# Kernel tuning notes

Hardware: AMD Instinct MI355X
Metric: run time of the kernel (lower is better)

## Reference

```python
import jax, jax.numpy as jnp
import numpy as np

B, S, V, D = 4, 2048, 50265, 768
H_LF, DH = 12, 64          # longformer-base heads
C, W = 256, 256            # chunk size, one-sided window
DFF = 3072
NH, DK = 4, 768            # outer MultiHeadAttention(n_head=4, d_k=d_v=768)


def layer_norm(x, g, b, eps=1e-5):
    mu = jnp.mean(x, axis=-1, keepdims=True)
    var = jnp.var(x, axis=-1, keepdims=True)
    return (x - mu) * jax.lax.rsqrt(var + eps) * g + b


def _overlap_chunks(t):
    # t: [B,H,S,dh] -> [B,H,nc,3c,dh] key blocks (chunks j-1,j,j+1, zero-padded at ends)
    nc = S // C
    tp = jnp.pad(t, ((0, 0), (0, 0), (C, C), (0, 0)))
    tr = tp.reshape(t.shape[0], t.shape[1], nc + 2, C, t.shape[-1])
    return jnp.concatenate([tr[:, :, :nc], tr[:, :, 1:nc + 1], tr[:, :, 2:]], axis=3)


def sliding_window_attn(q, k, v):
    # exact band attention: query i attends keys j with |i-j| <= W
    nc = S // C
    qc = q.reshape(q.shape[0], q.shape[1], nc, C, DH)
    kb = _overlap_chunks(k)
    vb = _overlap_chunks(v)
    scores = jnp.einsum('bhncd,bhnkd->bhnck', qc, kb) / np.sqrt(DH)
    ci = jnp.arange(C)[:, None]
    ki = jnp.arange(3 * C)[None, :]
    band = jnp.abs(ki - C - ci) <= W                      # [c,3c]
    n = jnp.arange(nc)[:, None]
    kpos = n * C - C + jnp.arange(3 * C)[None, :]
    valid = (kpos >= 0) & (kpos < S)                      # [nc,3c]
    mask = band[None, :, :] & valid[:, None, :]           # [nc,c,3c]
    scores = jnp.where(mask[None, None], scores, -1e9)
    a = jax.nn.softmax(scores, axis=-1)
    out = jnp.einsum('bhnck,bhnkd->bhncd', a, vb)
    return out.reshape(q.shape)


def longformer_layer(x, emb, pos, ln_e_g, ln_e_b, lf_wq, lf_wk, lf_wv, lf_wo,
                     ln1_g, ln1_b, w1, w2, ln2_g, ln2_b):
    h = layer_norm(emb[x] + pos[None], ln_e_g, ln_e_b)    # [B,S,D]
    def heads(w):
        return (h @ w).reshape(B, S, H_LF, DH).transpose(0, 2, 1, 3)
    q, k, v = heads(lf_wq), heads(lf_wk), heads(lf_wv)
    a = sliding_window_attn(q, k, v)                      # [B,H,S,dh]
    a = a.transpose(0, 2, 1, 3).reshape(B, S, D) @ lf_wo
    h = layer_norm(h + a, ln1_g, ln1_b)
    f = jax.nn.gelu(h @ w1) @ w2
    return layer_norm(h + f, ln2_g, ln2_b)


def mha_and_pool(x, out_lf, mha_wq, mha_wk, mha_wv, mha_fc, mha_ln_g, mha_ln_b):
    residual = out_lf
    def heads(w):
        return (out_lf @ w).reshape(B, S, NH, DK).transpose(0, 2, 1, 3)
    q, k, v = heads(mha_wq), heads(mha_wk), heads(mha_wv)
    scores = jnp.einsum('bhqd,bhkd->bhqk', q, k) / np.sqrt(DK)
    key_mask = (x != 0)[:, None, None, :]
    scores = jnp.where(key_mask, scores, -1e9)
    a = jax.nn.softmax(scores, axis=-1)
    o = jnp.einsum('bhqk,bhkd->bhqd', a, v)
    o = o.transpose(0, 2, 1, 3).reshape(B, S, NH * DK) @ mha_fc
    out_attn = layer_norm(o + residual, mha_ln_g, mha_ln_b)
    return jnp.max(out_attn, axis=1)                      # max_pool1d over seq -> [B,D]


def setup_inputs() -> dict:
    key = jax.random.key(0)
    ks = jax.random.split(key, 16)
    s = 0.02
    d = {
        'x': jax.random.randint(ks[0], (B, S), 0, V),
        'emb': jax.random.normal(ks[1], (V, D), jnp.float32) * s,
        'pos': jax.random.normal(ks[2], (S, D), jnp.float32) * s,
        'ln_e_g': jnp.ones((D,), jnp.float32), 'ln_e_b': jnp.zeros((D,), jnp.float32),
        'lf_wq': jax.random.normal(ks[3], (D, D), jnp.float32) * s,
        'lf_wk': jax.random.normal(ks[4], (D, D), jnp.float32) * s,
        'lf_wv': jax.random.normal(ks[5], (D, D), jnp.float32) * s,
        'lf_wo': jax.random.normal(ks[6], (D, D), jnp.float32) * s,
        'ln1_g': jnp.ones((D,), jnp.float32), 'ln1_b': jnp.zeros((D,), jnp.float32),
        'w1': jax.random.normal(ks[7], (D, DFF), jnp.float32) * s,
        'w2': jax.random.normal(ks[8], (DFF, D), jnp.float32) * s,
        'ln2_g': jnp.ones((D,), jnp.float32), 'ln2_b': jnp.zeros((D,), jnp.float32),
        'mha_wq': jax.random.normal(ks[9], (D, NH * DK), jnp.float32) * s,
        'mha_wk': jax.random.normal(ks[10], (D, NH * DK), jnp.float32) * s,
        'mha_wv': jax.random.normal(ks[11], (D, NH * DK), jnp.float32) * s,
        'mha_fc': jax.random.normal(ks[12], (NH * DK, D), jnp.float32) * s,
        'mha_ln_g': jnp.ones((D,), jnp.float32), 'mha_ln_b': jnp.zeros((D,), jnp.float32),
    }
    return d


def reference(x, emb, pos, ln_e_g, ln_e_b, lf_wq, lf_wk, lf_wv, lf_wo,
              ln1_g, ln1_b, w1, w2, ln2_g, ln2_b,
              mha_wq, mha_wk, mha_wv, mha_fc, mha_ln_g, mha_ln_b):
    out_lf = longformer_layer(x, emb, pos, ln_e_g, ln_e_b, lf_wq, lf_wk, lf_wv, lf_wo,
                              ln1_g, ln1_b, w1, w2, ln2_g, ln2_b)
    out_lf = jax.lax.stop_gradient(out_lf)  # torch.no_grad() around longformer
    return mha_and_pool(x, out_lf, mha_wq, mha_wk, mha_wv, mha_fc, mha_ln_g, mha_ln_b)
```

## Files before the change

### kernel.cpp

```cpp
#include <hip/hip_runtime.h>
#include <hip/hip_bf16.h>
#include <math.h>

#define DEV static __device__ __forceinline__

typedef unsigned short u16;
typedef __attribute__((ext_vector_type(8))) __bf16 bf16x8;
typedef __attribute__((ext_vector_type(8))) unsigned short u16x8;
typedef __attribute__((ext_vector_type(4))) unsigned short u16x4;
typedef __attribute__((ext_vector_type(4))) float f32x4;
typedef __attribute__((ext_vector_type(4))) int i32x4;

constexpr int SL  = 2048;
constexpr int DM  = 768;
constexpr int DH  = 64;
constexpr int DFF = 3072;
constexpr int DKM = 768;

DEV float b2f(u16 u){ union{float f; unsigned u;} c; c.u = ((unsigned)u)<<16; return c.f; }
DEV u16 f2b(float f){ union{float f; unsigned u;} c; c.f=f; unsigned r=(c.u + 0x7fffu + ((c.u>>16)&1u))>>16; return (u16)r; }

DEV void gld16(u16* lds, const u16* g){
  __builtin_amdgcn_global_load_lds((const __attribute__((address_space(1))) void*)g,
                                   (__attribute__((address_space(3))) void*)lds, 16, 0, 0);
}

DEV float wred_sum(float v){
#pragma unroll
  for (int o=32;o;o>>=1) v += __shfl_xor(v,o,64);
  return v;
}
DEV float wred_max(float v){
#pragma unroll
  for (int o=32;o;o>>=1) v = fmaxf(v, __shfl_xor(v,o,64));
  return v;
}
DEV float bred_sum(float v, float* sm){
  v = wred_sum(v);
  if ((threadIdx.x & 63)==0) sm[threadIdx.x>>6] = v;
  __syncthreads();
  float r = sm[0]+sm[1]+sm[2]+sm[3];
  __syncthreads();
  return r;
}

#define PHASE_SYNC \
  __builtin_amdgcn_s_barrier(); \
  asm volatile("s_waitcnt lgkmcnt(0)" ::: "memory"); \
  __builtin_amdgcn_sched_barrier(0); \
  __builtin_amdgcn_s_setprio(1);
#define PHASE_END \
  __builtin_amdgcn_s_setprio(0); \
  __builtin_amdgcn_s_barrier();

#define MFMA_PH(MH, NH) \
  { _Pragma("unroll") for (int mi2=0; mi2<4; ++mi2) { \
      _Pragma("unroll") for (int ni2=0; ni2<2; ++ni2) { \
        acc[(MH)*4+mi2][(NH)*2+ni2] = __builtin_amdgcn_mfma_f32_16x16x32_bf16(Af[mi2][0], Bf[(NH)*2+ni2][0], acc[(MH)*4+mi2][(NH)*2+ni2], 0,0,0); \
        acc[(MH)*4+mi2][(NH)*2+ni2] = __builtin_amdgcn_mfma_f32_16x16x32_bf16(Af[mi2][1], Bf[(NH)*2+ni2][1], acc[(MH)*4+mi2][(NH)*2+ni2], 0,0,0); } } }

template<int MODE, int EPI>
__global__ __launch_bounds__(512,2) void gemm256_k(
    const u16* __restrict__ A, const u16* __restrict__ Bt,
    float* __restrict__ Cf, u16* __restrict__ Cb,
    u16* __restrict__ Cb2, u16* __restrict__ Cb3,
    int K, int lda, int ldb, int ldc)
{
  extern __shared__ u16 lds_dyn[];
  const int tid = threadIdx.x, lane = tid & 63, wv = tid >> 6;
  const int wr = wv >> 2, wc = wv & 3;
  const int m0 = blockIdx.x * 256, n0 = blockIdx.y * 256, z = blockIdx.z;
  const int nt = K >> 6;

  int bb = 0, hh = 0;
  long long baseA = 0, baseB = 0;
  if constexpr (MODE==1) { bb=z>>2; hh=z&3; baseA=(long long)bb*SL*3072 + hh*DKM; baseB=baseA; }

  const int rb = (wv*64 + lane) >> 3;
  const int sg = ((lane & 7) ^ (rb & 7)) * 8;
  const int rd0 = (lane & 15)*64 + (((lane>>4) ^ (lane & 7)) * 8);
  const int rd1 = rd0 ^ 32;

  auto stageA = [&](int buf, int half, int kt) {
#pragma unroll
    for (int tt = 0; tt < 2; ++tt) {
      const int t = half + tt*2;
      gld16(lds_dyn + buf*16384 + t*4096 + wv*512,
            A + baseA + (long long)(m0 + t*64 + rb)*lda + (long long)kt*64 + sg);
    }
  };
  auto stageB = [&](int buf, int half, int kt) {
#pragma unroll
    for (int tt = 0; tt < 2; ++tt) {
      const int t = half*2 + tt;
      gld16(lds_dyn + 32768 + buf*16384 + t*4096 + wv*512,
            Bt + baseB + (long long)(n0 + t*64 + rb)*ldb + (long long)kt*64 + sg);
    }
  };

  f32x4 acc[8][4] = {};
  bf16x8 Af[4][2];
  bf16x8 Bf[4][2];

  stageA(0,0,0); stageB(0,0,0); stageB(0,1,0); stageA(0,1,0);
  stageA(1,0,1); stageB(1,0,1); stageB(1,1,1);
  asm volatile("s_waitcnt vmcnt(6)" ::: "memory");
  __builtin_amdgcn_s_barrier();

  for (int t = 0; t < nt; ++t) {
    const int d = t & 1;
    const u16* As_d = lds_dyn + d*16384;
    const u16* Bs_d = lds_dyn + 32768 + d*16384;
#pragma unroll
    for (int mi2=0; mi2<4; ++mi2) {
      const u16* p = As_d + (wr*128 + mi2*16)*64;
      Af[mi2][0] = *(const bf16x8*)(p + rd0);
      Af[mi2][1] = *(const bf16x8*)(p + rd1);
    }
#pragma unroll
    for (int ni2=0; ni2<2; ++ni2) {
      const u16* p = Bs_d + (wc*64 + ni2*16)*64;
      Bf[ni2][0] = *(const bf16x8*)(p + rd0);
      Bf[ni2][1] = *(const bf16x8*)(p + rd1);
    }
    if (t+1 < nt) stageA(d^1, 1, t+1);
    PHASE_SYNC; MFMA_PH(0,0); PHASE_END;
#pragma unroll
    for (int ni2=0; ni2<2; ++ni2) {
      const u16* p = Bs_d + (wc*64 + 32 + ni2*16)*64;
      Bf[2+ni2][0] = *(const bf16x8*)(p + rd0);
      Bf[2+ni2][1] = *(const bf16x8*)(p + rd1);
    }
    if (t+2 < nt) stageA(d, 0, t+2);
    PHASE_SYNC; MFMA_PH(0,1); PHASE_END;
#pragma unroll
    for (int mi2=0; mi2<4; ++mi2) {
      const u16* p = As_d + (wr*128 + 64 + mi2*16)*64;
      Af[mi2][0] = *(const bf16x8*)(p + rd0);
      Af[mi2][1] = *(const bf16x8*)(p + rd1);
    }
    if (t+2 < nt) stageB(d, 0, t+2);
    PHASE_SYNC; MFMA_PH(1,0); PHASE_END;
    if (t+2 < nt) stageB(d, 1, t+2);
    __builtin_amdgcn_s_barrier();
    __builtin_amdgcn_s_setprio(1);
    MFMA_PH(1,1);
    __builtin_amdgcn_s_setprio(0);
    if (t+2 < nt)      { asm volatile("s_waitcnt vmcnt(6)" ::: "memory"); }
    else if (t+1 < nt) { asm volatile("s_waitcnt vmcnt(0)" ::: "memory"); }
    __builtin_amdgcn_s_barrier();
  }

#pragma unroll
  for (int mi=0; mi<8; ++mi)
#pragma unroll
  for (int ni=0; ni<4; ++ni)
#pragma unroll
  for (int r=0; r<4; ++r) {
    int m = m0 + wr*128 + mi*16 + ((lane>>4)<<2) + r;
    int n = n0 + wc*64  + ni*16 + (lane & 15);
    float v = acc[mi][ni][r];
    if constexpr (EPI==2) {
      float u = 0.7978845608f*(v + 0.044715f*v*v*v);
      float th = 1.f - 2.f/(__expf(2.f*u)+1.f);
      v = 0.5f*v*(1.f + th);
    }
    if constexpr (EPI==3) v *= 0.0360843918f;
    if constexpr (MODE==3) {
      int seg = n / 3072, nn = n - seg*3072;
      u16* dst = seg==0 ? Cb : (seg==1 ? Cb2 : Cb3);
      dst[(long long)m*3072 + nn] = f2b(v);
    } else {
      long long ci;
      if constexpr (MODE==1) ci = (long long)z*SL*SL + (long long)m*SL + n;
      else                   ci = (long long)m*ldc + n;
      if constexpr (EPI==0) Cf[ci] = v; else Cb[ci] = f2b(v);
    }
  }
}

#define MFMA_Q(MB, NB, AF) \
  { _Pragma("unroll") for (int mi2=0; mi2<2; ++mi2) { \
      _Pragma("unroll") for (int ni2=0; ni2<2; ++ni2) { \
        acc[(MB)+mi2][(NB)+ni2] = __builtin_amdgcn_mfma_f32_16x16x32_bf16(AF[mi2][0], Bf[(NB)+ni2][0], acc[(MB)+mi2][(NB)+ni2], 0,0,0); \
        acc[(MB)+mi2][(NB)+ni2] = __builtin_amdgcn_mfma_f32_16x16x32_bf16(AF[mi2][1], Bf[(NB)+ni2][1], acc[(MB)+mi2][(NB)+ni2], 0,0,0); } } }

__global__ __launch_bounds__(512,2) void gemm128n_k(
    const u16* __restrict__ A, const u16* __restrict__ Bt, u16* __restrict__ Cb, int K)
{
  extern __shared__ u16 lds_dyn[];
  const int tid = threadIdx.x, lane = tid & 63, wv = tid >> 6;
  const int wr = wv >> 1, wc = wv & 1;
  const int m0 = blockIdx.x * 256, n0 = blockIdx.y * 128, z = blockIdx.z;
  const int bb = z >> 2, hh = z & 3;
  const long long baseA = (long long)z*SL*SL;
  const long long baseB = ((long long)bb*3072 + hh*DKM)*SL;
  const int nt = K >> 6;

  const int rb = (wv*64 + lane) >> 3;
  const int sg = ((lane & 7) ^ (rb & 7)) * 8;
  const int rd0 = (lane & 15)*64 + (((lane>>4) ^ (lane & 7)) * 8);
  const int rd1 = rd0 ^ 32;

  auto stageA = [&](int buf, int half, int kt) {
#pragma unroll
    for (int tt = 0; tt < 2; ++tt) {
      const int t = half*2 + tt;
      gld16(lds_dyn + buf*16384 + t*4096 + wv*512,
            A + baseA + (long long)(m0 + t*64 + rb)*SL + (long long)kt*64 + sg);
    }
  };
  auto stageB = [&](int buf, int idx, int kt) {
    gld16(lds_dyn + 32768 + buf*8192 + idx*4096 + wv*512,
          Bt + baseB + (long long)(n0 + idx*64 + rb)*SL + (long long)kt*64 + sg);
  };

  f32x4 acc[4][4] = {};
  bf16x8 Af[2][2];
  bf16x8 Bf[4][2];

  stageA(0,0,0); stageB(0,0,0); stageB(0,1,0); stageA(0,1,0);
  stageA(1,0,1); stageB(1,0,1); stageB(1,1,1);
  asm volatile("s_waitcnt vmcnt(4)" ::: "memory");
  __builtin_amdgcn_s_barrier();

  for (int t = 0; t < nt; ++t) {
    const int d = t & 1;
    const u16* As_d = lds_dyn + d*16384;
    const u16* Bs_d = lds_dyn + 32768 + d*8192;
#pragma unroll
    for (int mi2=0; mi2<2; ++mi2) {
      const u16* p = As_d + (wr*32 + mi2*16)*64;
      Af[mi2][0] = *(const bf16x8*)(p + rd0);
      Af[mi2][1] = *(const bf16x8*)(p + rd1);
    }
#pragma unroll
    for (int ni2=0; ni2<2; ++ni2) {
      const u16* p = Bs_d + (wc*64 + ni2*16)*64;
      Bf[ni2][0] = *(const bf16x8*)(p + rd0);
      Bf[ni2][1] = *(const bf16x8*)(p + rd1);
    }
    if (t+1 < nt) stageA(d^1, 1, t+1);
    PHASE_SYNC; MFMA_Q(0,0,Af); PHASE_END;
#pragma unroll
    for (int ni2=0; ni2<2; ++ni2) {
      const u16* p = Bs_d + (wc*64 + 32 + ni2*16)*64;
      Bf[2+ni2][0] = *(const bf16x8*)(p + rd0);
      Bf[2+ni2][1] = *(const bf16x8*)(p + rd1);
    }
    if (t+2 < nt) stageA(d, 0, t+2);
    PHASE_SYNC; MFMA_Q(0,2,Af); PHASE_END;
#pragma unroll
    for (int mi2=0; mi2<2; ++mi2) {
      const u16* p = As_d + (128 + wr*32 + mi2*16)*64;
      Af[mi2][0] = *(const bf16x8*)(p + rd0);
      Af[mi2][1] = *(const bf16x8*)(p + rd1);
    }
    if (t+2 < nt) stageB(d, 0, t+2);
    PHASE_SYNC; MFMA_Q(2,0,Af); PHASE_END;
    if (t+2 < nt) stageB(d, 1, t+2);
    __builtin_amdgcn_s_barrier();
    __builtin_amdgcn_s_setprio(1);
    MFMA_Q(2,2,Af);
    __builtin_amdgcn_s_setprio(0);
    if (t+2 < nt)      { asm volatile("s_waitcnt vmcnt(4)" ::: "memory"); }
    else if (t+1 < nt) { asm volatile("s_waitcnt vmcnt(0)" ::: "memory"); }
    __builtin_amdgcn_s_barrier();
  }

#pragma unroll
  for (int mi=0; mi<4; ++mi)
#pragma unroll
  for (int ni=0; ni<4; ++ni)
#pragma unroll
  for (int r=0; r<4; ++r) {
    int m = m0 + (mi>>1)*128 + wr*32 + (mi&1)*16 + ((lane>>4)<<2) + r;
    int n = n0 + wc*64 + ni*16 + (lane & 15);
    Cb[((long long)bb*SL + m)*3072 + hh*DKM + n] = f2b(acc[mi][ni][r]);
  }
}

template<int BM, int BN, int MODE, int EPI>
__global__ __launch_bounds__(256) void gemm_k(
    const u16* __restrict__ A, const u16* __restrict__ Bt,
    float* __restrict__ Cf, u16* __restrict__ Cb,
    u16* __restrict__ Cb2, u16* __restrict__ Cb3,
    int K, int lda, int ldb, int ldc)
{
  constexpr int BK = 32;
  constexpr int WM = BM/2, WN = BN/2, FM = WM/16, FN = WN/16;
  __shared__ __attribute__((aligned(16))) u16 As[BM*BK];
  __shared__ __attribute__((aligned(16))) u16 Bs[BN*BK];
  const int tid = threadIdx.x, lane = tid & 63, wv = tid >> 6;
  const int wr = wv >> 1, wc = wv & 1;
  const int m0 = blockIdx.x * BM, n0 = blockIdx.y * BN, z = blockIdx.z;

  int k_lo = 0, k_hi = K;
  if constexpr (MODE==6) { int kh = K >> 1; k_lo = z*kh; k_hi = k_lo + kh; }

  f32x4 acc[FM][FN] = {};

  for (int kt = k_lo; kt < k_hi; kt += BK) {
#pragma unroll
    for (int t = 0; t < (BM*4)/256; ++t) {
      int cb  = (t*4 + wv)*64;
      int ch  = cb + lane;
      int row = ch >> 2, cp = ch & 3;
      int gp  = cp ^ (row & 3) ^ ((row >> 2) & 1);
      long long ga = (long long)(m0 + row)*lda + (kt + gp*8);
      gld16(&As[cb*8], A + ga);
    }
#pragma unroll
    for (int t = 0; t < (BN*4)/256; ++t) {
      int cb  = (t*4 + wv)*64;
      int ch  = cb + lane;
      int row = ch >> 2, cp = ch & 3;
      int gp  = cp ^ (row & 3) ^ ((row >> 2) & 1);
      long long gb = (long long)(n0 + row)*ldb + (kt + gp*8);
      gld16(&Bs[cb*8], Bt + gb);
    }
    __syncthreads();
    bf16x8 af[FM], bfr[FN];
#pragma unroll
    for (int mi=0; mi<FM; ++mi) {
      int row = wr*WM + mi*16 + (lane & 15);
      int cp  = (lane >> 4) ^ (row & 3) ^ ((row >> 2) & 1);
      af[mi] = *reinterpret_cast<const bf16x8*>(&As[row*BK + cp*8]);
    }
#pragma unroll
    for (int ni=0; ni<FN; ++ni) {
      int row = wc*WN + ni*16 + (lane & 15);
      int cp  = (lane >> 4) ^ (row & 3) ^ ((row >> 2) & 1);
      bfr[ni] = *reinterpret_cast<const bf16x8*>(&Bs[row*BK + cp*8]);
    }
#pragma unroll
    for (int mi=0; mi<FM; ++mi)
#pragma unroll
      for (int ni=0; ni<FN; ++ni)
        acc[mi][ni] = __builtin_amdgcn_mfma_f32_16x16x32_bf16(af[mi], bfr[ni], acc[mi][ni], 0,0,0);
    __syncthreads();
  }

#pragma unroll
  for (int mi=0; mi<FM; ++mi)
#pragma unroll
  for (int ni=0; ni<FN; ++ni)
#pragma unroll
  for (int r=0; r<4; ++r) {
    int m = m0 + wr*WM + mi*16 + ((lane>>4)<<2) + r;
    int n = n0 + wc*WN + ni*16 + (lane & 15);
    float v = acc[mi][ni][r];
    if constexpr (MODE==5) {
      int seg = n / 768, nn = n - seg*768;
      u16* dst = seg==0 ? Cb : (seg==1 ? Cb2 : Cb3);
      dst[(long long)m*768 + nn] = f2b(v);
    } else if constexpr (MODE==6) {
      Cf[(long long)z*8192*ldc + (long long)m*ldc + n] = v;
    } else {
      long long ci = (long long)m*ldc + n;
      if constexpr (EPI==0) Cf[ci] = v; else Cb[ci] = f2b(v);
    }
  }
}

__global__ __launch_bounds__(256) void sw_attn_k(
    const u16* __restrict__ Qm, const u16* __restrict__ Km,
    const u16* __restrict__ Vt, u16* __restrict__ Om)
{
  __shared__ __attribute__((aligned(16))) u16 Kb_s[64*64];
  __shared__ __attribute__((aligned(16))) u16 Vb_s[64*64];
  __shared__ __attribute__((aligned(16))) u16 Pb_s[4*32*64];
  const int tid = threadIdx.x, lane = tid & 63, wv = tid >> 6;
  const int qc = blockIdx.x >> 1, half = blockIdx.x & 1;
  const int h = blockIdx.y, b = blockIdx.z;
  const int q0 = qc*256 + half*128 + wv*32;
  const long long rowbase = (long long)b*SL;

  bf16x8 Qf[2][2];
#pragma unroll
  for (int mi=0;mi<2;++mi)
#pragma unroll
    for (int ks=0;ks<2;++ks)
      Qf[mi][ks] = *(const bf16x8*)(Qm + (rowbase + q0 + mi*16 + (lane&15))*DM + h*DH + ks*32 + (lane>>4)*8);

  f32x4 accO[2][4] = {};
  float mrun[2][4], lrun[2][4];
#pragma unroll
  for (int mi=0;mi<2;++mi)
#pragma unroll
    for (int r=0;r<4;++r){ mrun[mi][r]=-3e38f; lrun[mi][r]=0.f; }

  const int srow = tid >> 3;
  const int schunk = (tid & 7) ^ (srow & 7);

  const int kb0 = qc*256 + half*128 - 256;
  const int slo = kb0 < 0 ? ((-kb0) >> 6) : 0;
  const int shi_t = (SL - kb0) >> 6;
  const int shi = shi_t < 10 ? shi_t : 10;

  const int qpb = q0 + ((lane>>4)<<2);

  for (int s = slo; s < shi; ++s) {
    const int kb = kb0 + s*64;
#pragma unroll
    for (int ii=0; ii<2; ++ii) {
      gld16(Kb_s + ii*2048 + wv*512,
            Km + (rowbase + kb + srow + ii*32)*DM + h*DH + schunk*8);
      gld16(Vb_s + ii*2048 + wv*512,
            Vt + ((long long)b*DM + h*DH + srow + ii*32)*SL + kb + schunk*8);
    }
    asm volatile("s_waitcnt vmcnt(0)" ::: "memory");
    __syncthreads();

    f32x4 accS[2][4] = {};
    {
      bf16x8 Kf[4][2];
#pragma unroll
      for (int nf=0;nf<4;++nf){
        int row = nf*16 + (lane&15);
#pragma unroll
        for (int ks=0;ks<2;++ks){
          int ch = ((lane>>4) + ks*4) ^ (row&7);
          Kf[nf][ks] = *(const bf16x8*)(Kb_s + row*64 + ch*8);
        }
      }
#pragma unroll
      for (int mi=0;mi<2;++mi)
#pragma unroll
        for (int nf=0;nf<4;++nf){
          accS[mi][nf] = __builtin_amdgcn_mfma_f32_16x16x32_bf16(Qf[mi][0], Kf[nf][0], accS[mi][nf], 0,0,0);
          accS[mi][nf] = __builtin_amdgcn_mfma_f32_16x16x32_bf16(Qf[mi][1], Kf[nf][1], accS[mi][nf], 0,0,0);
        }
    }

    float smax[2][4];
#pragma unroll
    for (int mi=0;mi<2;++mi)
#pragma unroll
      for (int r=0;r<4;++r) smax[mi][r] = -3e38f;
#pragma unroll
    for (int mi=0;mi<2;++mi)
#pragma unroll
      for (int nf=0;nf<4;++nf)
#pragma unroll
        for (int r=0;r<4;++r){
          int dd = (kb + nf*16 + (lane&15)) - (qpb + mi*16 + r);
          bool ok = (dd <= 256) && (dd >= -256);
          float v = ok ? accS[mi][nf][r]*0.125f : -3e38f;
          accS[mi][nf][r] = v;
          smax[mi][r] = fmaxf(smax[mi][r], v);
        }
#pragma unroll
    for (int mi=0;mi<2;++mi)
#pragma unroll
      for (int r=0;r<4;++r){
        float v = smax[mi][r];
        v = fmaxf(v, __shfl_xor(v,1,64)); v = fmaxf(v, __shfl_xor(v,2,64));
        v = fmaxf(v, __shfl_xor(v,4,64)); v = fmaxf(v, __shfl_xor(v,8,64));
        smax[mi][r] = v;
      }

#pragma unroll
    for (int mi=0;mi<2;++mi)
#pragma unroll
      for (int r=0;r<4;++r){
        float mn = fmaxf(mrun[mi][r], smax[mi][r]);
        float sc = __expf(mrun[mi][r] - mn);
        float ls = 0.f;
#pragma unroll
        for (int nf=0;nf<4;++nf){
          float sv = accS[mi][nf][r];
          float p = (sv > -1e37f) ? __expf(sv - mn) : 0.f;
          accS[mi][nf][r] = p;
          ls += p;
        }
        ls += __shfl_xor(ls,1,64); ls += __shfl_xor(ls,2,64);
        ls += __shfl_xor(ls,4,64); ls += __shfl_xor(ls,8,64);
        lrun[mi][r] = lrun[mi][r]*sc + ls;
        mrun[mi][r] = mn;
#pragma unroll
        for (int df=0;df<4;++df) accO[mi][df][r] *= sc;
      }
#pragma unroll
    for (int mi=0;mi<2;++mi)
#pragma unroll
      for (int nf=0;nf<4;++nf)
#pragma unroll
        for (int r=0;r<4;++r){
          int ql = mi*16 + ((lane>>4)<<2) + r;
          int k  = nf*16 + (lane&15);
          int ch = (k>>3) ^ (ql&7);
          Pb_s[wv*2048 + ql*64 + ch*8 + (k&7)] = f2b(accS[mi][nf][r]);
        }
    asm volatile("s_waitcnt lgkmcnt(0)" ::: "memory");
    __builtin_amdgcn_sched_barrier(0);

    {
      bf16x8 Pf[2][2], Vf[4][2];
#pragma unroll
      for (int mi=0;mi<2;++mi){
        int ql = mi*16 + (lane&15);
#pragma unroll
        for (int ks=0;ks<2;++ks){
          int ch = ((lane>>4) + ks*4) ^ (ql&7);
          Pf[mi][ks] = *(const bf16x8*)(Pb_s + wv*2048 + ql*64 + ch*8);
        }
      }
#pragma unroll
      for (int df=0;df<4;++df){
        int dr = df*16 + (lane&15);
#pragma unroll
        for (int ks=0;ks<2;++ks){
          int ch = ((lane>>4) + ks*4) ^ (dr&7);
          Vf[df][ks] = *(const bf16x8*)(Vb_s + dr*64 + ch*8);
        }
      }
#pragma unroll
      for (int mi=0;mi<2;++mi)
#pragma unroll
        for (int df=0;df<4;++df){
          accO[mi][df] = __builtin_amdgcn_mfma_f32_16x16x32_bf16(Pf[mi][0], Vf[df][0], accO[mi][df], 0,0,0);
          accO[mi][df] = __builtin_amdgcn_mfma_f32_16x16x32_bf16(Pf[mi][1], Vf[df][1], accO[mi][df], 0,0,0);
        }
    }
    __syncthreads();
  }

#pragma unroll
  for (int mi=0;mi<2;++mi)
#pragma unroll
    for (int df=0;df<4;++df)
#pragma unroll
      for (int r=0;r<4;++r){
        long long row = rowbase + qpb + mi*16 + r;
        int col = h*DH + df*16 + (lane&15);
        Om[row*DM + col] = f2b(accO[mi][df][r] / lrun[mi][r]);
      }
}

__global__ __launch_bounds__(256) void embed_ln_k(const int* __restrict__ x,
    const float* __restrict__ emb, const float* __restrict__ pos,
    const float* __restrict__ g, const float* __restrict__ bta,
    float* __restrict__ of, u16* __restrict__ ob)
{
  __shared__ float sm[4];
  const int row = blockIdx.x, s = row & (SL-1);
  const long long tok = x[row];
  const float* e = emb + tok*DM;
  const float* p = pos + (long long)s*DM;
  float v[3], su=0.f, sq=0.f;
#pragma unroll
  for (int i=0;i<3;++i){ int d=threadIdx.x+i*256; v[i]=e[d]+p[d]; su+=v[i]; sq+=v[i]*v[i]; }
  su = bred_sum(su, sm); sq = bred_sum(sq, sm);
  float mean = su*(1.f/DM), var = sq*(1.f/DM)-mean*mean, rs = rsqrtf(var+1e-5f);
#pragma unroll
  for (int i=0;i<3;++i){ int d=threadIdx.x+i*256;
    float o = (v[i]-mean)*rs*g[d] + bta[d];
    of[(long long)row*DM+d]=o; ob[(long long)row*DM+d]=f2b(o); }
}

__global__ __launch_bounds__(256) void resid_ln_k(const float* __restrict__ a, const float* __restrict__ c,
    const float* __restrict__ c2,
    const float* __restrict__ g, const float* __restrict__ bta,
    float* __restrict__ of, u16* __restrict__ ob)
{
  __shared__ float sm[4];
  const long long row = blockIdx.x;
  const float* ra = a + row*DM;
  const float* rc = c + row*DM;
  float v[3], su=0.f, sq=0.f;
#pragma unroll
  for (int i=0;i<3;++i){
    int d=threadIdx.x+i*256;
    v[i]=ra[d]+rc[d];
    if (c2) v[i]+=c2[row*DM+d];
    su+=v[i]; sq+=v[i]*v[i];
  }
  su = bred_sum(su, sm); sq = bred_sum(sq, sm);
  float mean = su*(1.f/DM), var = sq*(1.f/DM)-mean*mean, rs = rsqrtf(var+1e-5f);
#pragma unroll
  for (int i=0;i<3;++i){ int d=threadIdx.x+i*256;
    float o = (v[i]-mean)*rs*g[d] + bta[d];
    of[row*DM+d]=o; if (ob) ob[row*DM+d]=f2b(o); }
}

__global__ __launch_bounds__(256) void transp_w_k(const float* __restrict__ W, u16* __restrict__ Wt, int Kd, int Nd)
{
  __shared__ float t[64][65];
  int n0 = blockIdx.x*64, k0 = blockIdx.y*64;
  int lx = threadIdx.x & 15, ly = threadIdx.x >> 4;
#pragma unroll
  for (int i=0;i<4;++i){
    const float4 v = *(const float4*)(W + (long long)(k0+ly+i*16)*Nd + n0 + lx*4);
    t[ly+i*16][lx*4+0]=v.x; t[ly+i*16][lx*4+1]=v.y; t[ly+i*16][lx*4+2]=v.z; t[ly+i*16][lx*4+3]=v.w;
  }
  __syncthreads();
#pragma unroll
  for (int i=0;i<4;++i){
    int nn = ly + i*16, kk = lx*4;
    u16x4 o = { f2b(t[kk][nn]), f2b(t[kk+1][nn]), f2b(t[kk+2][nn]), f2b(t[kk+3][nn]) };
    *(u16x4*)(Wt + (long long)(n0+nn)*Kd + k0 + kk) = o;
  }
}

__global__ __launch_bounds__(256) void transp_b_k(const u16* __restrict__ in, u16* __restrict__ out, int Nc)
{
  __shared__ u16 t[32][33];
  int c0 = blockIdx.x*32, r0 = blockIdx.y*32;
  int lx = threadIdx.x & 31, ly = threadIdx.x >> 5;
#pragma unroll
  for (int i=0;i<4;++i) t[ly+i*8][lx] = in[(long long)(r0+ly+i*8)*Nc + c0+lx];
  __syncthreads();
  int b = r0 >> 11, s0 = r0 & (SL-1);
#pragma unroll
  for (int i=0;i<4;++i) out[((long long)b*Nc + c0+ly+i*8)*SL + s0+lx] = t[lx][ly+i*8];
}

__global__ __launch_bounds__(256) void mha_softmax_k(u16* __restrict__ sc, const int* __restrict__ x)
{
  const int r = blockIdx.x*4 + (threadIdx.x >> 6);
  const int lane = threadIdx.x & 63;
  const int z = r >> 11;
  const int b = z >> 2;
  u16* row = sc + (long long)z*SL*SL + (long long)(r & (SL-1))*SL;
  const int* xb = x + b*SL;
  float v[32]; float mx = -3e38f;
#pragma unroll
  for (int i=0;i<4;++i){
    const int j0 = i*512 + lane*8;
    u16x8 pv = *(const u16x8*)(row + j0);
    i32x4 xa = *(const i32x4*)(xb + j0);
    i32x4 xc = *(const i32x4*)(xb + j0 + 4);
#pragma unroll
    for (int e=0;e<8;++e){
      int xv = e<4 ? xa[e] : xc[e-4];
      float f = (xv != 0) ? b2f(pv[e]) : -3e38f;
      v[i*8+e] = f;
      mx = fmaxf(mx, f);
    }
  }
  mx = wred_max(mx);
  float s = 0.f;
#pragma unroll
  for (int i=0;i<32;++i){ v[i] = (v[i] > -1e37f) ? __expf(v[i]-mx) : 0.f; s += v[i]; }
  s = wred_sum(s);
  float inv = 1.f/s;
#pragma unroll
  for (int i=0;i<4;++i){
    u16x8 ov;
#pragma unroll
    for (int e=0;e<8;++e) ov[e] = f2b(v[i*8+e]*inv);
    *(u16x8*)(row + i*512 + lane*8) = ov;
  }
}

__global__ __launch_bounds__(256) void pool_part_k(const float* __restrict__ f, float* __restrict__ pp)
{
  int b = blockIdx.x, ch = blockIdx.y;
  float m0=-3e38f, m1=-3e38f, m2=-3e38f;
  for (int s = ch*32; s < ch*32+32; ++s){
    const float* r = f + ((long long)b*SL + s)*DM;
    m0=fmaxf(m0,r[threadIdx.x]); m1=fmaxf(m1,r[threadIdx.x+256]); m2=fmaxf(m2,r[threadIdx.x+512]);
  }
  float* o = pp + (long long)(b*64+ch)*DM;
  o[threadIdx.x]=m0; o[threadIdx.x+256]=m1; o[threadIdx.x+512]=m2;
}

__global__ __launch_bounds__(256) void pool_red_k(const float* __restrict__ pp, float* __restrict__ out)
{
  int b = blockIdx.x;
#pragma unroll
  for (int i=0;i<3;++i){
    int d = threadIdx.x + i*256;
    float m = -3e38f;
    for (int c=0;c<64;++c) m = fmaxf(m, pp[(long long)(b*64+c)*DM + d]);
    out[(long long)b*DM + d] = m;
  }
}

extern "C" void kernel_launch(void* const* d_in, const int* in_sizes, int n_in,
                              void* d_out, int out_size, void* d_ws, size_t ws_size,
                              hipStream_t stream)
{
  const int*   x      = (const int*)  d_in[0];
  const float* emb    = (const float*)d_in[1];
  const float* pos    = (const float*)d_in[2];
  const float* ln_e_g = (const float*)d_in[3];
  const float* ln_e_b = (const float*)d_in[4];
  const float* lf_wq  = (const float*)d_in[5];
  const float* lf_wk  = (const float*)d_in[6];
  const float* lf_wv  = (const float*)d_in[7];
  const float* lf_wo  = (const float*)d_in[8];
  const float* ln1_g  = (const float*)d_in[9];
  const float* ln1_b  = (const float*)d_in[10];
  const float* w1     = (const float*)d_in[11];
  const float* w2     = (const float*)d_in[12];
  const float* ln2_g  = (const float*)d_in[13];
  const float* ln2_b  = (const float*)d_in[14];
  const float* mha_wq = (const float*)d_in[15];
  const float* mha_wk = (const float*)d_in[16];
  const float* mha_wv = (const float*)d_in[17];
  const float* mha_fc = (const float*)d_in[18];
  const float* mha_ln_g = (const float*)d_in[19];
  const float* mha_ln_b = (const float*)d_in[20];

  (void)hipFuncSetAttribute((const void*)gemm256_k<0,2>, hipFuncAttributeMaxDynamicSharedMemorySize, 131072);
  (void)hipFuncSetAttribute((const void*)gemm256_k<1,3>, hipFuncAttributeMaxDynamicSharedMemorySize, 131072);
  (void)hipFuncSetAttribute((const void*)gemm256_k<3,1>, hipFuncAttributeMaxDynamicSharedMemorySize, 131072);
  (void)hipFuncSetAttribute((const void*)gemm128n_k,     hipFuncAttributeMaxDynamicSharedMemorySize, 98304);

  const long long R = 8192;
  float* F0 = (float*)d_ws;
  float* F1 = F0 + R*DM;
  float* F2 = F1 + R*DM;
  u16* B0 = (u16*)(F2 + R*DM);
  u16* B1 = B0 + R*DM;
  u16* B2 = B1 + R*DM;
  u16* B3 = B2 + R*DM;
  u16* WT = B3 + R*DM;
  u16* G1 = WT + (long long)9216*DM;
  u16* G2 = G1 + R*DFF;
  u16* G3 = G2 + R*DFF;
  u16* SC = G3 + R*DFF;
  float* FS = (float*)SC;
  float* PP = (float*)(SC + (long long)16*SL*SL);

  dim3 T(256), T5(512);
  const size_t SM256 = 131072, SM128 = 98304;

  embed_ln_k<<<dim3(8192), T, 0, stream>>>(x, emb, pos, ln_e_g, ln_e_b, F0, B0);

  transp_w_k<<<dim3(12,12), T, 0, stream>>>(lf_wq, WT,               DM, DM);
  transp_w_k<<<dim3(12,12), T, 0, stream>>>(lf_wk, WT + 768*768,     DM, DM);
  transp_w_k<<<dim3(12,12), T, 0, stream>>>(lf_wv, WT + 2*768*768,   DM, DM);
  gemm_k<128,128,5,1><<<dim3(64,18), T, 0, stream>>>(B0, WT, nullptr, B1, B2, SC, DM, DM, DM, 0);
  transp_b_k<<<dim3(24,256), T, 0, stream>>>(SC, B3, DM);

  sw_attn_k<<<dim3(16,12,4), T, 0, stream>>>(B1, B2, B3, B0);

  transp_w_k<<<dim3(12,12), T, 0, stream>>>(lf_wo, WT, DM, DM);
  gemm_k<128,128,6,0><<<dim3(64,6,2), T, 0, stream>>>(B0, WT, FS, nullptr, nullptr, nullptr, DM, DM, DM, DM);
  resid_ln_k<<<dim3(8192), T, 0, stream>>>(F0, FS, FS + R*DM, ln1_g, ln1_b, F2, B1);

  transp_w_k<<<dim3(48,12), T, 0, stream>>>(w1, WT, DM, DFF);
  gemm256_k<0,2><<<dim3(32,12,1), T5, SM256, stream>>>(B1, WT, nullptr, G1, nullptr, nullptr, DM, DM, DM, DFF);
  transp_w_k<<<dim3(12,48), T, 0, stream>>>(w2, WT, DFF, DM);
  gemm_k<128,128,6,0><<<dim3(64,6,2), T, 0, stream>>>(G1, WT, FS, nullptr, nullptr, nullptr, DFF, DFF, DFF, DM);
  resid_ln_k<<<dim3(8192), T, 0, stream>>>(F2, FS, FS + R*DM, ln2_g, ln2_b, F0, B2);

  transp_w_k<<<dim3(48,12), T, 0, stream>>>(mha_wq, WT,                 DM, DFF);
  transp_w_k<<<dim3(48,12), T, 0, stream>>>(mha_wk, WT + (long long)3072*768, DM, DFF);
  transp_w_k<<<dim3(48,12), T, 0, stream>>>(mha_wv, WT + (long long)6144*768, DM, DFF);
  gemm256_k<3,1><<<dim3(32,36,1), T5, SM256, stream>>>(B2, WT, nullptr, G1, G2, SC, DM, DM, DM, 0);
  transp_b_k<<<dim3(96,256), T, 0, stream>>>(SC, G3, DFF);

  gemm256_k<1,3><<<dim3(8,8,16), T5, SM256, stream>>>(G1, G2, nullptr, SC, nullptr, nullptr, DKM, 3072, 3072, 0);
  mha_softmax_k<<<dim3(8192), T, 0, stream>>>(SC, x);
  gemm128n_k<<<dim3(8,6,16), T5, SM128, stream>>>(SC, G3, G2, SL);

  transp_w_k<<<dim3(12,48), T, 0, stream>>>(mha_fc, WT, DFF, DM);
  gemm_k<128,128,6,0><<<dim3(64,6,2), T, 0, stream>>>(G2, WT, FS, nullptr, nullptr, nullptr, DFF, DFF, DFF, DM);
  resid_ln_k<<<dim3(8192), T, 0, stream>>>(F0, FS, FS + R*DM, mha_ln_g, mha_ln_b, F2, nullptr);

  pool_part_k<<<dim3(4,64), T, 0, stream>>>(F2, PP);
  pool_red_k<<<dim3(4), T, 0, stream>>>(PP, (float*)d_out);
}
```

Before: 936.2 us.

## Use 256x128 GEMM for FFN/QKV and drop split-K on N=768 GEMMs

Result: no change. 953.5 us (+1.9%).

```diff
diff --git a/kernel.cpp b/kernel.cpp
--- a/kernel.cpp
+++ b/kernel.cpp
@@ -63,7 +63,6 @@
 __global__ __launch_bounds__(512,2) void gemm256_k(
     const u16* __restrict__ A, const u16* __restrict__ Bt,
     float* __restrict__ Cf, u16* __restrict__ Cb,
-    u16* __restrict__ Cb2, u16* __restrict__ Cb3,
     int K, int lda, int ldb, int ldc)
 {
   extern __shared__ u16 lds_dyn[];
@@ -160,22 +159,11 @@
     int m = m0 + wr*128 + mi*16 + ((lane>>4)<<2) + r;
     int n = n0 + wc*64  + ni*16 + (lane & 15);
     float v = acc[mi][ni][r];
-    if constexpr (EPI==2) {
-      float u = 0.7978845608f*(v + 0.044715f*v*v*v);
-      float th = 1.f - 2.f/(__expf(2.f*u)+1.f);
-      v = 0.5f*v*(1.f + th);
-    }
     if constexpr (EPI==3) v *= 0.0360843918f;
-    if constexpr (MODE==3) {
-      int seg = n / 3072, nn = n - seg*3072;
-      u16* dst = seg==0 ? Cb : (seg==1 ? Cb2 : Cb3);
-      dst[(long long)m*3072 + nn] = f2b(v);
-    } else {
-      long long ci;
-      if constexpr (MODE==1) ci = (long long)z*SL*SL + (long long)m*SL + n;
-      else                   ci = (long long)m*ldc + n;
-      if constexpr (EPI==0) Cf[ci] = v; else Cb[ci] = f2b(v);
-    }
+    long long ci;
+    if constexpr (MODE==1) ci = (long long)z*SL*SL + (long long)m*SL + n;
+    else                   ci = (long long)m*ldc + n;
+    if constexpr (EPI==0) Cf[ci] = v; else Cb[ci] = f2b(v);
   }
 }
 
@@ -185,16 +173,20 @@
         acc[(MB)+mi2][(NB)+ni2] = __builtin_amdgcn_mfma_f32_16x16x32_bf16(AF[mi2][0], Bf[(NB)+ni2][0], acc[(MB)+mi2][(NB)+ni2], 0,0,0); \
         acc[(MB)+mi2][(NB)+ni2] = __builtin_amdgcn_mfma_f32_16x16x32_bf16(AF[mi2][1], Bf[(NB)+ni2][1], acc[(MB)+mi2][(NB)+ni2], 0,0,0); } } }
 
+template<int MODE, int EPI>
 __global__ __launch_bounds__(512,2) void gemm128n_k(
-    const u16* __restrict__ A, const u16* __restrict__ Bt, u16* __restrict__ Cb, int K)
+    const u16* __restrict__ A, const u16* __restrict__ Bt,
+    u16* __restrict__ Cb, u16* __restrict__ Cb2, u16* __restrict__ Cb3,
+    int K, int lda, int ldb, int ldc)
 {
   extern __shared__ u16 lds_dyn[];
   const int tid = threadIdx.x, lane = tid & 63, wv = tid >> 6;
   const int wr = wv >> 1, wc = wv & 1;
   const int m0 = blockIdx.x * 256, n0 = blockIdx.y * 128, z = blockIdx.z;
-  const int bb = z >> 2, hh = z & 3;
-  const long long baseA = (long long)z*SL*SL;
-  const long long baseB = ((long long)bb*3072 + hh*DKM)*SL;
+  int bb = 0, hh = 0;
+  long long baseA = 0, baseB = 0;
+  if constexpr (MODE==2) { bb = z >> 2; hh = z & 3;
+    baseA = (long long)z*SL*SL; baseB = ((long long)bb*3072 + hh*DKM)*SL; }
   const int nt = K >> 6;
 
   const int rb = (wv*64 + lane) >> 3;
@@ -207,12 +199,12 @@
     for (int tt = 0; tt < 2; ++tt) {
       const int t = half*2 + tt;
       gld16(lds_dyn + buf*16384 + t*4096 + wv*512,
-            A + baseA + (long long)(m0 + t*64 + rb)*SL + (long long)kt*64 + sg);
+            A + baseA + (long long)(m0 + t*64 + rb)*lda + (long long)kt*64 + sg);
     }
   };
   auto stageB = [&](int buf, int idx, int kt) {
     gld16(lds_dyn + 32768 + buf*8192 + idx*4096 + wv*512,
-          Bt + baseB + (long long)(n0 + idx*64 + rb)*SL + (long long)kt*64 + sg);
+          Bt + baseB + (long long)(n0 + idx*64 + rb)*ldb + (long long)kt*64 + sg);
   };
 
   f32x4 acc[4][4] = {};
@@ -276,7 +268,21 @@
   for (int r=0; r<4; ++r) {
     int m = m0 + (mi>>1)*128 + wr*32 + (mi&1)*16 + ((lane>>4)<<2) + r;
     int n = n0 + wc*64 + ni*16 + (lane & 15);
-    Cb[((long long)bb*SL + m)*3072 + hh*DKM + n] = f2b(acc[mi][ni][r]);
+    float v = acc[mi][ni][r];
+    if constexpr (EPI==2) {
+      float u = 0.7978845608f*(v + 0.044715f*v*v*v);
+      float th = 1.f - 2.f/(__expf(2.f*u)+1.f);
+      v = 0.5f*v*(1.f + th);
+    }
+    if constexpr (MODE==2) {
+      Cb[((long long)bb*SL + m)*3072 + hh*DKM + n] = f2b(v);
+    } else if constexpr (MODE==3) {
+      int seg = n / 3072, nn = n - seg*3072;
+      u16* dst = seg==0 ? Cb : (seg==1 ? Cb2 : Cb3);
+      dst[(long long)m*3072 + nn] = f2b(v);
+    } else {
+      Cb[(long long)m*ldc + n] = f2b(v);
+    }
   }
 }
 
@@ -293,14 +299,11 @@
   __shared__ __attribute__((aligned(16))) u16 Bs[BN*BK];
   const int tid = threadIdx.x, lane = tid & 63, wv = tid >> 6;
   const int wr = wv >> 1, wc = wv & 1;
-  const int m0 = blockIdx.x * BM, n0 = blockIdx.y * BN, z = blockIdx.z;
-
-  int k_lo = 0, k_hi = K;
-  if constexpr (MODE==6) { int kh = K >> 1; k_lo = z*kh; k_hi = k_lo + kh; }
+  const int m0 = blockIdx.x * BM, n0 = blockIdx.y * BN;
 
   f32x4 acc[FM][FN] = {};
 
-  for (int kt = k_lo; kt < k_hi; kt += BK) {
+  for (int kt = 0; kt < K; kt += BK) {
 #pragma unroll
     for (int t = 0; t < (BM*4)/256; ++t) {
       int cb  = (t*4 + wv)*64;
@@ -354,8 +357,6 @@
       int seg = n / 768, nn = n - seg*768;
       u16* dst = seg==0 ? Cb : (seg==1 ? Cb2 : Cb3);
       dst[(long long)m*768 + nn] = f2b(v);
-    } else if constexpr (MODE==6) {
-      Cf[(long long)z*8192*ldc + (long long)m*ldc + n] = v;
     } else {
       long long ci = (long long)m*ldc + n;
       if constexpr (EPI==0) Cf[ci] = v; else Cb[ci] = f2b(v);
@@ -560,7 +561,6 @@
 }
 
 __global__ __launch_bounds__(256) void resid_ln_k(const float* __restrict__ a, const float* __restrict__ c,
-    const float* __restrict__ c2,
     const float* __restrict__ g, const float* __restrict__ bta,
     float* __restrict__ of, u16* __restrict__ ob)
 {
@@ -573,7 +573,6 @@
   for (int i=0;i<3;++i){
     int d=threadIdx.x+i*256;
     v[i]=ra[d]+rc[d];
-    if (c2) v[i]+=c2[row*DM+d];
     su+=v[i]; sq+=v[i]*v[i];
   }
   su = bred_sum(su, sm); sq = bred_sum(sq, sm);
@@ -704,10 +703,10 @@
   const float* mha_ln_g = (const float*)d_in[19];
   const float* mha_ln_b = (const float*)d_in[20];
 
-  (void)hipFuncSetAttribute((const void*)gemm256_k<0,2>, hipFuncAttributeMaxDynamicSharedMemorySize, 131072);
-  (void)hipFuncSetAttribute((const void*)gemm256_k<1,3>, hipFuncAttributeMaxDynamicSharedMemorySize, 131072);
-  (void)hipFuncSetAttribute((const void*)gemm256_k<3,1>, hipFuncAttributeMaxDynamicSharedMemorySize, 131072);
-  (void)hipFuncSetAttribute((const void*)gemm128n_k,     hipFuncAttributeMaxDynamicSharedMemorySize, 98304);
+  (void)hipFuncSetAttribute((const void*)gemm256_k<1,3>,  hipFuncAttributeMaxDynamicSharedMemorySize, 131072);
+  (void)hipFuncSetAttribute((const void*)gemm128n_k<0,2>, hipFuncAttributeMaxDynamicSharedMemorySize, 98304);
+  (void)hipFuncSetAttribute((const void*)gemm128n_k<2,1>, hipFuncAttributeMaxDynamicSharedMemorySize, 98304);
+  (void)hipFuncSetAttribute((const void*)gemm128n_k<3,1>, hipFuncAttributeMaxDynamicSharedMemorySize, 98304);
 
   const long long R = 8192;
   float* F0 = (float*)d_ws;
@@ -722,7 +721,6 @@
   u16* G2 = G1 + R*DFF;
   u16* G3 = G2 + R*DFF;
   u16* SC = G3 + R*DFF;
-  float* FS = (float*)SC;
   float* PP = (float*)(SC + (long long)16*SL*SL);
 
   dim3 T(256), T5(512);
@@ -739,28 +737,28 @@
   sw_attn_k<<<dim3(16,12,4), T, 0, stream>>>(B1, B2, B3, B0);
 
   transp_w_k<<<dim3(12,12), T, 0, stream>>>(lf_wo, WT, DM, DM);
-  gemm_k<128,128,6,0><<<dim3(64,6,2), T, 0, stream>>>(B0, WT, FS, nullptr, nullptr, nullptr, DM, DM, DM, DM);
-  resid_ln_k<<<dim3(8192), T, 0, stream>>>(F0, FS, FS + R*DM, ln1_g, ln1_b, F2, B1);
+  gemm_k<128,128,0,0><<<dim3(64,6), T, 0, stream>>>(B0, WT, F1, nullptr, nullptr, nullptr, DM, DM, DM, DM);
+  resid_ln_k<<<dim3(8192), T, 0, stream>>>(F0, F1, ln1_g, ln1_b, F2, B1);
 
   transp_w_k<<<dim3(48,12), T, 0, stream>>>(w1, WT, DM, DFF);
-  gemm256_k<0,2><<<dim3(32,12,1), T5, SM256, stream>>>(B1, WT, nullptr, G1, nullptr, nullptr, DM, DM, DM, DFF);
+  gemm128n_k<0,2><<<dim3(32,24,1), T5, SM128, stream>>>(B1, WT, G1, nullptr, nullptr, DM, DM, DM, DFF);
   transp_w_k<<<dim3(12,48), T, 0, stream>>>(w2, WT, DFF, DM);
-  gemm_k<128,128,6,0><<<dim3(64,6,2), T, 0, stream>>>(G1, WT, FS, nullptr, nullptr, nullptr, DFF, DFF, DFF, DM);
-  resid_ln_k<<<dim3(8192), T, 0, stream>>>(F2, FS, FS + R*DM, ln2_g, ln2_b, F0, B2);
+  gemm_k<128,128,0,0><<<dim3(64,6), T, 0, stream>>>(G1, WT, F1, nullptr, nullptr, nullptr, DFF, DFF, DFF, DM);
+  resid_ln_k<<<dim3(8192), T, 0, stream>>>(F2, F1, ln2_g, ln2_b, F0, B2);
 
   transp_w_k<<<dim3(48,12), T, 0, stream>>>(mha_wq, WT,                 DM, DFF);
   transp_w_k<<<dim3(48,12), T, 0, stream>>>(mha_wk, WT + (long long)3072*768, DM, DFF);
   transp_w_k<<<dim3(48,12), T, 0, stream>>>(mha_wv, WT + (long long)6144*768, DM, DFF);
-  gemm256_k<3,1><<<dim3(32,36,1), T5, SM256, stream>>>(B2, WT, nullptr, G1, G2, SC, DM, DM, DM, 0);
+  gemm128n_k<3,1><<<dim3(32,72,1), T5, SM128, stream>>>(B2, WT, G1, G2, SC, DM, DM, DM, 0);
   transp_b_k<<<dim3(96,256), T, 0, stream>>>(SC, G3, DFF);
 
-  gemm256_k<1,3><<<dim3(8,8,16), T5, SM256, stream>>>(G1, G2, nullptr, SC, nullptr, nullptr, DKM, 3072, 3072, 0);
+  gemm256_k<1,3><<<dim3(8,8,16), T5, SM256, stream>>>(G1, G2, nullptr, SC, DKM, 3072, 3072, 0);
   mha_softmax_k<<<dim3(8192), T, 0, stream>>>(SC, x);
-  gemm128n_k<<<dim3(8,6,16), T5, SM128, stream>>>(SC, G3, G2, SL);
+  gemm128n_k<2,1><<<dim3(8,6,16), T5, SM128, stream>>>(SC, G3, G2, nullptr, nullptr, SL, SL, SL, 0);
 
   transp_w_k<<<dim3(12,48), T, 0, stream>>>(mha_fc, WT, DFF, DM);
-  gemm_k<128,128,6,0><<<dim3(64,6,2), T, 0, stream>>>(G2, WT, FS, nullptr, nullptr, nullptr, DFF, DFF, DFF, DM);
-  resid_ln_k<<<dim3(8192), T, 0, stream>>>(F0, FS, FS + R*DM, mha_ln_g, mha_ln_b, F2, nullptr);
+  gemm_k<128,128,0,0><<<dim3(64,6), T, 0, stream>>>(G2, WT, F1, nullptr, nullptr, nullptr, DFF, DFF, DFF, DM);
+  resid_ln_k<<<dim3(8192), T, 0, stream>>>(F0, F1, mha_ln_g, mha_ln_b, F2, nullptr);
 
   pool_part_k<<<dim3(4,64), T, 0, stream>>>(F2, PP);
   pool_red_k<<<dim3(4), T, 0, stream>>>(PP, (float*)d_out);
```

## Replace split-K N=768 GEMMs with 128x64 tiles and remap big-GEMM block order

Applied to the files above, without the earlier changes.

Result: no change. 953.3 us (+1.8%).

```diff
diff --git a/kernel.cpp b/kernel.cpp
--- a/kernel.cpp
+++ b/kernel.cpp
@@ -69,7 +69,13 @@
   extern __shared__ u16 lds_dyn[];
   const int tid = threadIdx.x, lane = tid & 63, wv = tid >> 6;
   const int wr = wv >> 2, wc = wv & 3;
-  const int m0 = blockIdx.x * 256, n0 = blockIdx.y * 256, z = blockIdx.z;
+  int bx = blockIdx.x, by = blockIdx.y;
+  if constexpr (MODE==0 || MODE==3) {
+    const int gy = gridDim.y;
+    const int k8 = bx & 7, j = (bx >> 3) + 4*by;
+    bx = k8*4 + j/gy;  by = j - (j/gy)*gy;
+  }
+  const int m0 = bx * 256, n0 = by * 256, z = blockIdx.z;
   const int nt = K >> 6;
 
   int bb = 0, hh = 0;
@@ -293,14 +299,11 @@
   __shared__ __attribute__((aligned(16))) u16 Bs[BN*BK];
   const int tid = threadIdx.x, lane = tid & 63, wv = tid >> 6;
   const int wr = wv >> 1, wc = wv & 1;
-  const int m0 = blockIdx.x * BM, n0 = blockIdx.y * BN, z = blockIdx.z;
-
-  int k_lo = 0, k_hi = K;
-  if constexpr (MODE==6) { int kh = K >> 1; k_lo = z*kh; k_hi = k_lo + kh; }
+  const int m0 = blockIdx.x * BM, n0 = blockIdx.y * BN;
 
   f32x4 acc[FM][FN] = {};
 
-  for (int kt = k_lo; kt < k_hi; kt += BK) {
+  for (int kt = 0; kt < K; kt += BK) {
 #pragma unroll
     for (int t = 0; t < (BM*4)/256; ++t) {
       int cb  = (t*4 + wv)*64;
@@ -354,8 +357,6 @@
       int seg = n / 768, nn = n - seg*768;
       u16* dst = seg==0 ? Cb : (seg==1 ? Cb2 : Cb3);
       dst[(long long)m*768 + nn] = f2b(v);
-    } else if constexpr (MODE==6) {
-      Cf[(long long)z*8192*ldc + (long long)m*ldc + n] = v;
     } else {
       long long ci = (long long)m*ldc + n;
       if constexpr (EPI==0) Cf[ci] = v; else Cb[ci] = f2b(v);
@@ -560,7 +561,6 @@
 }
 
 __global__ __launch_bounds__(256) void resid_ln_k(const float* __restrict__ a, const float* __restrict__ c,
-    const float* __restrict__ c2,
     const float* __restrict__ g, const float* __restrict__ bta,
     float* __restrict__ of, u16* __restrict__ ob)
 {
@@ -573,7 +573,6 @@
   for (int i=0;i<3;++i){
     int d=threadIdx.x+i*256;
     v[i]=ra[d]+rc[d];
-    if (c2) v[i]+=c2[row*DM+d];
     su+=v[i]; sq+=v[i]*v[i];
   }
   su = bred_sum(su, sm); sq = bred_sum(sq, sm);
@@ -722,7 +721,6 @@
   u16* G2 = G1 + R*DFF;
   u16* G3 = G2 + R*DFF;
   u16* SC = G3 + R*DFF;
-  float* FS = (float*)SC;
   float* PP = (float*)(SC + (long long)16*SL*SL);
 
   dim3 T(256), T5(512);
@@ -739,14 +737,14 @@
   sw_attn_k<<<dim3(16,12,4), T, 0, stream>>>(B1, B2, B3, B0);
 
   transp_w_k<<<dim3(12,12), T, 0, stream>>>(lf_wo, WT, DM, DM);
-  gemm_k<128,128,6,0><<<dim3(64,6,2), T, 0, stream>>>(B0, WT, FS, nullptr, nullptr, nullptr, DM, DM, DM, DM);
-  resid_ln_k<<<dim3(8192), T, 0, stream>>>(F0, FS, FS + R*DM, ln1_g, ln1_b, F2, B1);
+  gemm_k<128,64,0,0><<<dim3(64,12), T, 0, stream>>>(B0, WT, F1, nullptr, nullptr, nullptr, DM, DM, DM, DM);
+  resid_ln_k<<<dim3(8192), T, 0, stream>>>(F0, F1, ln1_g, ln1_b, F2, B1);
 
   transp_w_k<<<dim3(48,12), T, 0, stream>>>(w1, WT, DM, DFF);
   gemm256_k<0,2><<<dim3(32,12,1), T5, SM256, stream>>>(B1, WT, nullptr, G1, nullptr, nullptr, DM, DM, DM, DFF);
   transp_w_k<<<dim3(12,48), T, 0, stream>>>(w2, WT, DFF, DM);
-  gemm_k<128,128,6,0><<<dim3(64,6,2), T, 0, stream>>>(G1, WT, FS, nullptr, nullptr, nullptr, DFF, DFF, DFF, DM);
-  resid_ln_k<<<dim3(8192), T, 0, stream>>>(F2, FS, FS + R*DM, ln2_g, ln2_b, F0, B2);
+  gemm_k<128,64,0,0><<<dim3(64,12), T, 0, stream>>>(G1, WT, F1, nullptr, nullptr, nullptr, DFF, DFF, DFF, DM);
+  resid_ln_k<<<dim3(8192), T, 0, stream>>>(F2, F1, ln2_g, ln2_b, F0, B2);
 
   transp_w_k<<<dim3(48,12), T, 0, stream>>>(mha_wq, WT,                 DM, DFF);
   transp_w_k<<<dim3(48,12), T, 0, stream>>>(mha_wk, WT + (long long)3072*768, DM, DFF);
@@ -759,8 +757,8 @@
   gemm128n_k<<<dim3(8,6,16), T5, SM128, stream>>>(SC, G3, G2, SL);
 
   transp_w_k<<<dim3(12,48), T, 0, stream>>>(mha_fc, WT, DFF, DM);
-  gemm_k<128,128,6,0><<<dim3(64,6,2), T, 0, stream>>>(G2, WT, FS, nullptr, nullptr, nullptr, DFF, DFF, DFF, DM);
-  resid_ln_k<<<dim3(8192), T, 0, stream>>>(F0, FS, FS + R*DM, mha_ln_g, mha_ln_b, F2, nullptr);
+  gemm_k<128,64,0,0><<<dim3(64,12), T, 0, stream>>>(G2, WT, F1, nullptr, nullptr, nullptr, DFF, DFF, DFF, DM);
+  resid_ln_k<<<dim3(8192), T, 0, stream>>>(F0, F1, mha_ln_g, mha_ln_b, F2, nullptr);
 
   pool_part_k<<<dim3(4,64), T, 0, stream>>>(F2, PP);
   pool_red_k<<<dim3(4), T, 0, stream>>>(PP, (float*)d_out);
```
